# Kernel tuning notes

Measured on AMD Instinct MI355X. Metric: run time of the kernel, lower is better.

## Reference

```python
import jax, jax.numpy as jnp
import numpy as np

K = 3            # kernel size (hard-coded in CANCRB_Down: conv 3x3, stride 1, pad 1)
PAD = 1
S_CLUSTERS = 32  # cluster_num
KMEANS_ITERS = 8 # fixed Lloyd iterations (jit-friendly stand-in for the repo's kmeans)


def extract_patches(x):
    # x [B,C,H,W] -> [B,C,9,H,W] (3x3 neighborhoods, zero pad 1) == F.unfold layout
    B, C, H, W = x.shape
    xp = jnp.pad(x, ((0, 0), (0, 0), (PAD, PAD), (PAD, PAD)))
    return jnp.stack([xp[:, :, i:i + H, j:j + W] for i in range(K) for j in range(K)], axis=2)


def setup_inputs() -> dict:
    key = jax.random.key(0)
    ks = jax.random.split(key, 6)
    B, C, H, W = 8, 64, 128, 128
    O = C
    return {
        "x": jax.random.normal(ks[0], (B, C, H, W), jnp.float32),
        # LAGConv2D params: per-pixel 3x3 kernel-attention conv + base weight
        "att_w": jax.random.normal(ks[1], (K * K, C, K, K), jnp.float32) * 0.05,
        "att_b": jnp.zeros((K * K,), jnp.float32),
        "w1": jax.random.normal(ks[2], (O, C, K, K), jnp.float32) * (1.0 / np.sqrt(C * K * K)),
        "b1": jnp.zeros((O,), jnp.float32),
        # CANConv params: kernel generator (centroid patch -> 3x3 spatial attention) + base weight
        "kg_w": jax.random.normal(ks[3], (K * K, C * K * K), jnp.float32) * 0.02,
        "kg_b": jnp.zeros((K * K,), jnp.float32),
        "w2": jax.random.normal(ks[4], (O, C, K * K), jnp.float32) * (1.0 / np.sqrt(C * K * K)),
        "b2": jnp.zeros((O,), jnp.float32),
    }


def _lagconv(x, att_w, att_b, w1, b1):
    # local adaptive gating conv: per-pixel k*k attention modulates the shared kernel
    att = jax.nn.sigmoid(
        jax.lax.conv_general_dilated(x, att_w, (1, 1), "SAME") + att_b[None, :, None, None]
    )  # [B,9,H,W]
    p = extract_patches(x)  # [B,C,9,H,W]
    O, C = w1.shape[0], w1.shape[1]
    y = jnp.einsum('bckhw,bkhw,ock->bohw', p, att, w1.reshape(O, C, K * K))
    return y + b1[None, :, None, None]


def _kmeans_assign(feat, cent):
    # feat [B,N,C], cent [B,S,C] -> idx [B,N]; drop the ||feat||^2 constant
    d = jnp.sum(cent * cent, axis=-1)[:, None, :] - 2.0 * jnp.einsum('bnc,bsc->bns', feat, cent)
    return jnp.argmin(d, axis=-1)


def _kmeans(feat, S):
    B, N, C = feat.shape
    cent = feat[:, ::max(N // S, 1), :][:, :S, :]  # deterministic evenly-spaced init
    for _ in range(KMEANS_ITERS):
        idx = _kmeans_assign(feat, cent)
        oh = jax.nn.one_hot(idx, S, dtype=feat.dtype)          # [B,N,S]
        cnt = jnp.clip(jnp.sum(oh, axis=1), 1.0)               # [B,S]
        cent = jnp.einsum('bns,bnc->bsc', oh, feat) / cnt[..., None]
    return _kmeans_assign(feat, cent)


def _canconv(x, kg_w, kg_b, w2, b2, S):
    B, C, H, W = x.shape
    N = H * W
    feat = x.reshape(B, C, N).transpose(0, 2, 1)               # per-pixel channel features
    idx = _kmeans(feat, S)                                     # [B,N] cluster assignment
    p = extract_patches(x).reshape(B, C * K * K, N).transpose(0, 2, 1)  # [B,N,C*9]
    oh = jax.nn.one_hot(idx, S, dtype=x.dtype)
    cnt = jnp.clip(jnp.sum(oh, axis=1), 1.0)
    cent_p = jnp.einsum('bns,bnp->bsp', oh, p) / cnt[..., None]         # cluster mean patches
    # per-cluster 3x3 spatial attention; scaled softmax keeps kernel magnitude ~ base weight
    att = jax.nn.softmax(cent_p @ kg_w.T + kg_b, axis=-1) * float(K * K)  # [B,S,9]
    a_pix = jnp.take_along_axis(att, idx[..., None], axis=1)             # gather: [B,N,9]
    pm = p.reshape(B, N, C, K * K) * a_pix[:, :, None, :]
    y = jnp.einsum('bnck,ock->bno', pm, w2) + b2                          # [B,N,O]
    return y.transpose(0, 2, 1).reshape(B, w2.shape[0], H, W), idx


def reference(x, att_w, att_b, w1, b1, kg_w, kg_b, w2, b2):
    # NOTE: original torch forward overwrites `res` -- conv1+relu output is discarded.
    # We compute it for FLOP parity but it does not affect the output (faithful to the bug).
    _dead = jax.nn.relu(_lagconv(x, att_w, att_b, w1, b1))
    res, idx = _canconv(x, kg_w, kg_b, w2, b2, S_CLUSTERS)
    out = x + res
    return out, idx
```

## Files before the change

kernel.cpp:

```cpp
#include <hip/hip_runtime.h>
#include <hip/hip_bf16.h>

#define Bn 8
#define Cn 64
#define Np 16384
#define Sc 32
#define On 64
#define Dd 576
#define KM_ITERS 8
#define KMB 64
#define KBLK 32

typedef float f32x4 __attribute__((ext_vector_type(4)));
typedef __bf16 bf16x8 __attribute__((ext_vector_type(8)));
typedef __bf16 bf16x4 __attribute__((ext_vector_type(4)));

__device__ __forceinline__ void split3(float v, __bf16& h, __bf16& m, __bf16& lo) {
    h = (__bf16)v;
    float r = v - (float)h;
    m = (__bf16)r;
    lo = (__bf16)(r - (float)m);
}

__device__ __forceinline__ void split2(float v, __bf16& h, __bf16& m) {
    h = (__bf16)v;
    m = (__bf16)(v - (float)h);
}

__global__ __launch_bounds__(256) void featbf4_k(const float* __restrict__ x,
                                                 __bf16* __restrict__ fh,
                                                 __bf16* __restrict__ fm,
                                                 __bf16* __restrict__ xh,
                                                 __bf16* __restrict__ xm,
                                                 __bf16* __restrict__ xl) {
    __shared__ float tile[64][65];
    int b = blockIdx.y, n0 = blockIdx.x * 64, t = threadIdx.x;
    int j = t & 63, c0 = (t >> 6) * 16;
    #pragma unroll
    for (int cc = 0; cc < 16; ++cc)
        tile[c0 + cc][j] = x[((size_t)b * Cn + c0 + cc) * Np + n0 + j];
    __syncthreads();

    {
        int n_loc = t & 63, cq = (t >> 6) * 16;
        bf16x8 vh[2], vm[2];
        #pragma unroll
        for (int g = 0; g < 2; ++g)
            #pragma unroll
            for (int u = 0; u < 8; ++u) {
                __bf16 h, m;
                split2(tile[cq + g * 8 + u][n_loc], h, m);
                vh[g][u] = h; vm[g][u] = m;
            }
        size_t base = ((size_t)b * Np + n0 + n_loc) * Cn + cq;
        *(bf16x8*)&fh[base] = vh[0]; *(bf16x8*)&fh[base + 8] = vh[1];
        *(bf16x8*)&fm[base] = vm[0]; *(bf16x8*)&fm[base + 8] = vm[1];
    }
    {
        int c = t >> 2, jq = (t & 3) * 16;
        bf16x8 hh[2], mm2[2], ll[2];
        #pragma unroll
        for (int g = 0; g < 2; ++g)
            #pragma unroll
            for (int u = 0; u < 8; ++u) {
                __bf16 h, m, lo;
                split3(tile[c][jq + g * 8 + u], h, m, lo);
                hh[g][u] = h; mm2[g][u] = m; ll[g][u] = lo;
            }
        size_t cb = ((size_t)b * Cn + c) * Np + n0 + jq;
        *(bf16x8*)&xh[cb] = hh[0]; *(bf16x8*)&xh[cb + 8] = hh[1];
        *(bf16x8*)&xm[cb] = mm2[0]; *(bf16x8*)&xm[cb + 8] = mm2[1];
        *(bf16x8*)&xl[cb] = ll[0]; *(bf16x8*)&xl[cb + 8] = ll[1];
    }
}

__global__ __launch_bounds__(64) void init_cent3_k(const float* __restrict__ x,
                                                   float* __restrict__ cent_f32,
                                                   __bf16* __restrict__ ch_,
                                                   __bf16* __restrict__ cm_,
                                                   float* __restrict__ cnorm) {
    int b = blockIdx.y, s = blockIdx.x, c = threadIdx.x;
    int n = s * (Np / Sc);
    float v = x[((size_t)b * Cn + c) * Np + n];
    int o = (b * Sc + s) * Cn + c;
    cent_f32[o] = v;
    __bf16 h, m; split2(v, h, m);
    ch_[o] = h; cm_[o] = m;
    float sq = v * v;
    #pragma unroll
    for (int off = 32; off >= 1; off >>= 1) sq += __shfl_down(sq, off);
    if (c == 0) cnorm[b * Sc + s] = sq;
}

__global__ __launch_bounds__(256) void w2prep_k(const float* __restrict__ w2,
                                                __bf16* __restrict__ w2kg) {
    int i = blockIdx.x * 256 + threadIdx.x;
    int k = i >> 12, rem = i & 4095, o = rem >> 6, c = rem & 63;
    w2kg[i] = (__bf16)w2[o * Dd + c * 9 + k];
}

__global__ __launch_bounds__(256, 3) void kmeans_fused4_k(
        const float* __restrict__ x,
        const __bf16* __restrict__ fh, const __bf16* __restrict__ fm,
        const __bf16* __restrict__ xh, const __bf16* __restrict__ xm, const __bf16* __restrict__ xl,
        const float* __restrict__ cent_f32,
        const __bf16* __restrict__ ch_, const __bf16* __restrict__ cm_,
        const float* __restrict__ cnorm,
        int* __restrict__ idxg, float* __restrict__ gpart,
        float* __restrict__ out_idx, int do_update) {
    __shared__ __bf16 A_oh[32][264];
    __shared__ int idx_s[256];
    __shared__ int redint[4][32];
    __shared__ float centf_s[32][64];
    __shared__ float cnorm_s[32];
    int b = blockIdx.y, n0 = blockIdx.x * 256, t = threadIdx.x;
    int w = t >> 6, l = t & 63, arow = l & 15, kg = l >> 4;

    for (int i = t; i < Sc * Cn; i += 256) ((float*)centf_s)[i] = cent_f32[b * Sc * Cn + i];
    if (t < Sc) cnorm_s[t] = cnorm[b * Sc + t];

    bf16x8 cbh[2][2], cbm[2][2];
    #pragma unroll
    for (int st = 0; st < 2; ++st)
        #pragma unroll
        for (int kt = 0; kt < 2; ++kt) {
            size_t cb = (size_t)(b * Sc + st * 16 + arow) * Cn + kt * 32 + kg * 8;
            cbh[st][kt] = *(const bf16x8*)&ch_[cb];
            cbm[st][kt] = *(const bf16x8*)&cm_[cb];
        }
    float cn0 = cnorm[b * Sc + arow];
    float cn1 = cnorm[b * Sc + 16 + arow];

    f32x4 dacc[4][2];
    #pragma unroll
    for (int mt = 0; mt < 4; ++mt) {
        dacc[mt][0] = (f32x4){0.f, 0.f, 0.f, 0.f};
        dacc[mt][1] = (f32x4){0.f, 0.f, 0.f, 0.f};
    }
    #pragma unroll
    for (int mt = 0; mt < 4; ++mt) {
        size_t fb = ((size_t)b * Np + n0 + w * 64 + mt * 16 + arow) * Cn;
        bf16x8 ah[2], am2[2];
        #pragma unroll
        for (int kt = 0; kt < 2; ++kt) {
            ah[kt]  = *(const bf16x8*)&fh[fb + kt * 32 + kg * 8];
            am2[kt] = *(const bf16x8*)&fm[fb + kt * 32 + kg * 8];
        }
        #pragma unroll
        for (int st = 0; st < 2; ++st)
            #pragma unroll
            for (int kt = 0; kt < 2; ++kt) {
                dacc[mt][st] = __builtin_amdgcn_mfma_f32_16x16x32_bf16(ah[kt],  cbh[st][kt], dacc[mt][st], 0, 0, 0);
                dacc[mt][st] = __builtin_amdgcn_mfma_f32_16x16x32_bf16(ah[kt],  cbm[st][kt], dacc[mt][st], 0, 0, 0);
                dacc[mt][st] = __builtin_amdgcn_mfma_f32_16x16x32_bf16(am2[kt], cbh[st][kt], dacc[mt][st], 0, 0, 0);
                dacc[mt][st] = __builtin_amdgcn_mfma_f32_16x16x32_bf16(am2[kt], cbm[st][kt], dacc[mt][st], 0, 0, 0);
            }
    }
    __syncthreads();

    #pragma unroll
    for (int mt = 0; mt < 4; ++mt)
        #pragma unroll
        for (int r = 0; r < 4; ++r) {
            float dA = cn0 - 2.f * dacc[mt][0][r];
            float dB = cn1 - 2.f * dacc[mt][1][r];
            float d1, d2; int s1;
            if (dB < dA) { d1 = dB; s1 = arow + 16; d2 = dA; }
            else         { d1 = dA; s1 = arow;      d2 = dB; }
            #pragma unroll
            for (int mk = 1; mk < 16; mk <<= 1) {
                float d1o = __shfl_xor(d1, mk);
                int   s1o = __shfl_xor(s1, mk);
                float d2o = __shfl_xor(d2, mk);
                float big = fmaxf(d1, d1o);
                d2 = fminf(fminf(d2, d2o), big);
                if (d1o < d1 || (d1o == d1 && s1o < s1)) { d1 = d1o; s1 = s1o; }
            }
            int pix = w * 64 + mt * 16 + kg * 4 + r;
            bool writer = (arow == 0);
            if (writer) idx_s[pix] = s1;
            bool flag = writer && ((d2 - d1) < 0.02f);
            unsigned long long bal = __ballot(flag);
            while (bal) {
                int src = __ffsll(bal) - 1;
                bal &= bal - 1;
                int fp = w * 64 + mt * 16 + (src >> 4) * 4 + r;
                int n = n0 + fp;
                int s = l & 31, c0 = (l >> 5) * 32;
                float acc2 = 0.f;
                #pragma unroll 8
                for (int c = 0; c < 32; ++c)
                    acc2 = fmaf(x[((size_t)b * Cn + c0 + c) * Np + n], centf_s[s][c0 + c], acc2);
                acc2 += __shfl_xor(acc2, 32);
                float dd = cnorm_s[s] - 2.f * acc2;
                int ss = s;
                #pragma unroll
                for (int mk = 1; mk < 32; mk <<= 1) {
                    float ddo = __shfl_xor(dd, mk);
                    int   sso = __shfl_xor(ss, mk);
                    if (ddo < dd || (ddo == dd && sso < ss)) { dd = ddo; ss = sso; }
                }
                if (l == 0) idx_s[fp] = ss;
            }
        }
    __syncthreads();

    int best = idx_s[t];
    if (out_idx) {
        idxg[b * Np + n0 + t] = best;
        out_idx[b * Np + n0 + t] = (float)best;
    }
    if (!do_update) return;

    #pragma unroll 4
    for (int s = 0; s < Sc; ++s) {
        unsigned long long bal = __ballot(best == s);
        if (l == 0) redint[w][s] = __popcll(bal);
    }

    #pragma unroll
    for (int s = 0; s < Sc; ++s)
        A_oh[s][t] = (s == best) ? (__bf16)1.0f : (__bf16)0.0f;
    __syncthreads();

    f32x4 uacc[2];
    uacc[0] = (f32x4){0.f, 0.f, 0.f, 0.f};
    uacc[1] = (f32x4){0.f, 0.f, 0.f, 0.f};
    size_t xrow = ((size_t)b * Cn + (w * 16 + arow)) * Np + n0;
    for (int mc = 0; mc < 4; ++mc) {
        #pragma unroll
        for (int kh = 0; kh < 2; ++kh) {
            size_t off = xrow + mc * 64 + kh * 32 + kg * 8;
            bf16x8 bh  = *(const bf16x8*)&xh[off];
            bf16x8 bm2 = *(const bf16x8*)&xm[off];
            bf16x8 bl2 = *(const bf16x8*)&xl[off];
            #pragma unroll
            for (int smt = 0; smt < 2; ++smt) {
                bf16x8 af = *(const bf16x8*)&A_oh[smt * 16 + arow][mc * 64 + kh * 32 + kg * 8];
                uacc[smt] = __builtin_amdgcn_mfma_f32_16x16x32_bf16(af, bh,  uacc[smt], 0, 0, 0);
                uacc[smt] = __builtin_amdgcn_mfma_f32_16x16x32_bf16(af, bm2, uacc[smt], 0, 0, 0);
                uacc[smt] = __builtin_amdgcn_mfma_f32_16x16x32_bf16(af, bl2, uacc[smt], 0, 0, 0);
            }
        }
    }
    float* gp = &gpart[(size_t)(b * KMB + blockIdx.x) * (Sc * 65)];
    #pragma unroll
    for (int smt = 0; smt < 2; ++smt)
        #pragma unroll
        for (int r = 0; r < 4; ++r)
            gp[(smt * 16 + kg * 4 + r) * 65 + w * 16 + arow] = uacc[smt][r];
    if (t < Sc)
        gp[t * 65 + 64] = (float)(redint[0][t] + redint[1][t] + redint[2][t] + redint[3][t]);
}

__global__ __launch_bounds__(256) void update_reduce3_k(const float* __restrict__ gpart,
                                                        float* __restrict__ cent_f32,
                                                        __bf16* __restrict__ ch_,
                                                        __bf16* __restrict__ cm_,
                                                        float* __restrict__ cnorm) {
    __shared__ float psum[4][64];
    __shared__ float pcnt[4];
    int b = blockIdx.y, s = blockIdx.x, t = threadIdx.x;
    int w = t >> 6, c = t & 63;
    float sum = 0.f, cnt = 0.f;
    #pragma unroll 4
    for (int blk = w * 16; blk < w * 16 + 16; ++blk) {
        const float* g = &gpart[(size_t)(b * KMB + blk) * (Sc * 65) + s * 65];
        sum += g[c];
        if (c == 0) cnt += g[64];
    }
    psum[w][c] = sum;
    if (c == 0) pcnt[w] = cnt;
    __syncthreads();
    if (t < 64) {
        float m = psum[0][t] + psum[1][t] + psum[2][t] + psum[3][t];
        float ct = pcnt[0] + pcnt[1] + pcnt[2] + pcnt[3];
        float mean = m / fmaxf(ct, 1.f);
        int o = (b * Sc + s) * Cn + t;
        cent_f32[o] = mean;
        __bf16 h, mm; split2(mean, h, mm);
        ch_[o] = h; cm_[o] = mm;
        float sq = mean * mean;
        #pragma unroll
        for (int off = 32; off >= 1; off >>= 1) sq += __shfl_down(sq, off);
        if (t == 0) cnorm[b * Sc + s] = sq;
    }
}

__global__ __launch_bounds__(512) void centp_mfma2_k(const __bf16* __restrict__ xh,
                                                     const int* __restrict__ idxg,
                                                     float* __restrict__ partialP) {
    __shared__ __bf16 Amat[288 * 56];
    int b = blockIdx.y, kb = blockIdx.x, t = threadIdx.x;
    int w = t >> 6, l = t & 63;
    int wm = w >> 2, wn = w & 3;
    int arow = l & 15, kg = l >> 4;
    f32x4 acc[9];
    #pragma unroll
    for (int j = 0; j < 9; ++j) acc[j] = (f32x4){0.f, 0.f, 0.f, 0.f};

    int m_base = kb * 512;
    size_t xrow = ((size_t)b * Cn + wn * 16 + arow) * Np;
    for (int kt = 0; kt < 16; ++kt) {
        int m0 = m_base + kt * 32;
        #pragma unroll
        for (int j = 0; j < 9; ++j) {
            int i = t + 512 * j;
            int row = i >> 4, dc = i & 15;
            *(unsigned*)&Amat[row * 56 + dc * 2] = 0u;
        }
        __syncthreads();
        if (t < 288) {
            int m = t & 31, k = t >> 5;
            int mg = m0 + m, mh = mg >> 7, mw = mg & 127;
            int dh = k / 3 - 1, dw = k % 3 - 1;
            int nh = mh - dh, nw = mw - dw;
            if (((unsigned)nh < 128u) && ((unsigned)nw < 128u)) {
                int s = idxg[b * Np + (nh << 7) + nw];
                Amat[(s * 9 + k) * 56 + m] = (__bf16)1.0f;
            }
        }
        __syncthreads();
        bf16x8 bfrag = *(const bf16x8*)&xh[xrow + m0 + kg * 8];
        #pragma unroll
        for (int j = 0; j < 9; ++j) {
            int mt = wm * 9 + j;
            bf16x8 afrag = *(const bf16x8*)&Amat[(mt * 16 + arow) * 56 + kg * 8];
            acc[j] = __builtin_amdgcn_mfma_f32_16x16x32_bf16(afrag, bfrag, acc[j], 0, 0, 0);
        }
        __syncthreads();
    }
    float* P = partialP + (size_t)(b * KBLK + kb) * 288 * 64;
    #pragma unroll
    for (int j = 0; j < 9; ++j) {
        int R0 = (wm * 9 + j) * 16 + kg * 4;
        int col = wn * 16 + arow;
        #pragma unroll
        for (int r = 0; r < 4; ++r) P[(size_t)(R0 + r) * 64 + col] = acc[j][r];
    }
}

__global__ __launch_bounds__(576) void centp_att2_k(const float* __restrict__ partialP,
                                                    const int* __restrict__ idxg,
                                                    const float* __restrict__ kg_w,
                                                    const float* __restrict__ kg_b,
                                                    float* __restrict__ attb) {
    __shared__ float cpm[9][64];
    __shared__ float logit[9];
    __shared__ int   redint[9];
    __shared__ float cnt_sh;
    int b = blockIdx.y, s = blockIdx.x, t = threadIdx.x;
    int k = t >> 6, c = t & 63;

    float sum = 0.f;
    for (int kb = 0; kb < KBLK; ++kb)
        sum += partialP[((size_t)(b * KBLK + kb) * 288 + s * 9 + k) * 64 + c];

    int cloc = 0;
    for (int i = t; i < Np; i += 576) cloc += (idxg[b * Np + i] == s);
    #pragma unroll
    for (int off = 32; off >= 1; off >>= 1) cloc += __shfl_down(cloc, off);
    if ((t & 63) == 0) redint[k] = cloc;
    __syncthreads();
    if (t == 0) {
        int c2 = 0;
        #pragma unroll
        for (int j = 0; j < 9; ++j) c2 += redint[j];
        cnt_sh = fmaxf((float)c2, 1.f);
    }
    __syncthreads();
    cpm[k][c] = sum / cnt_sh;
    __syncthreads();

    float pr = 0.f;
    #pragma unroll
    for (int u = 0; u < 9; ++u)
        pr = fmaf(cpm[u][c], kg_w[k * Dd + c * 9 + u], pr);
    #pragma unroll
    for (int off = 32; off >= 1; off >>= 1) pr += __shfl_down(pr, off);
    if ((t & 63) == 0) logit[k] = pr + kg_b[k];
    __syncthreads();
    if (t == 0) {
        float mx = logit[0];
        #pragma unroll
        for (int jj = 1; jj < 9; ++jj) mx = fmaxf(mx, logit[jj]);
        float e[9], sm = 0.f;
        #pragma unroll
        for (int jj = 0; jj < 9; ++jj) { e[jj] = expf(logit[jj] - mx); sm += e[jj]; }
        #pragma unroll
        for (int jj = 0; jj < 9; ++jj) attb[(b * Sc + s) * 9 + jj] = e[jj] / sm * 9.f;
    }
}

__global__ __launch_bounds__(512, 4) void final_out5_k(const float* __restrict__ x,
                                                       const __bf16* __restrict__ fh,
                                                       const int* __restrict__ idxg,
                                                       const float* __restrict__ attb,
                                                       const __bf16* __restrict__ w2kg,
                                                       const float* __restrict__ b2,
                                                       float* __restrict__ out) {
    __shared__ __align__(16) char smem[46080];
    __shared__ float apix_t[9][132];
    __shared__ float b2s[64];
    __bf16 (*w2l)[64][72] = (__bf16 (*)[64][72])smem;
    float (*trans)[132]   = (float (*)[132])smem;

    int b = blockIdx.y, hh = blockIdx.x, n0 = hh * 128, t = threadIdx.x;
    int w = t >> 6, l = t & 63, arow = l & 15, kg = l >> 4;

    if (t < 128) {
        int s = idxg[b * Np + n0 + t];
        const float* ap = attb + (b * Sc + s) * 9;
        #pragma unroll
        for (int k = 0; k < 9; ++k) apix_t[k][t] = ap[k];
    } else if (t < 192) {
        b2s[t - 128] = b2[t - 128];
    }
    for (int q = t; q < 2560; q += 512) {
        int kk = q >> 9, rem = q & 511, o = rem >> 3, c0 = (rem & 7) * 8;
        *(bf16x8*)&w2l[kk][o][c0] = *(const bf16x8*)&w2kg[(size_t)kk * 4096 + o * 64 + c0];
    }
    __syncthreads();

    int px = w * 16 + arow;
    f32x4 acc[4];
    #pragma unroll
    for (int nt = 0; nt < 4; ++nt) acc[nt] = (f32x4){0.f, 0.f, 0.f, 0.f};

    #define K_BODY(k, kk)                                                                  \
    {                                                                                      \
        const int dh = (k) / 3 - 1, dw = (k) % 3 - 1;                                      \
        int h2 = hh + dh, wc = px + dw;                                                    \
        bool valid = ((unsigned)h2 < 128u) && ((unsigned)wc < 128u);                       \
        const __bf16* fr = fh + (((size_t)b * Np + (h2 << 7) + wc) << 6);                  \
        bf16x8 av0 = (bf16x8)(__bf16)0.0f, av1 = (bf16x8)(__bf16)0.0f;                     \
        if (valid) {                                                                       \
            av0 = *(const bf16x8*)&fr[kg * 8];                                             \
            av1 = *(const bf16x8*)&fr[32 + kg * 8];                                        \
        }                                                                                  \
        f32x4 a4 = *(const f32x4*)&apix_t[k][w * 16 + kg * 4];                             \
        f32x4 acck[4];                                                                     \
        _Pragma("unroll")                                                                  \
        for (int nt = 0; nt < 4; ++nt) {                                                   \
            bf16x8 bv0 = *(const bf16x8*)&w2l[kk][nt * 16 + arow][kg * 8];                 \
            bf16x8 bv1 = *(const bf16x8*)&w2l[kk][nt * 16 + arow][32 + kg * 8];            \
            acck[nt] = __builtin_amdgcn_mfma_f32_16x16x32_bf16(av0, bv0,                   \
                           (f32x4){0.f, 0.f, 0.f, 0.f}, 0, 0, 0);                          \
            acck[nt] = __builtin_amdgcn_mfma_f32_16x16x32_bf16(av1, bv1, acck[nt], 0, 0, 0);\
        }                                                                                  \
        _Pragma("unroll")                                                                  \
        for (int nt = 0; nt < 4; ++nt)                                                     \
            _Pragma("unroll")                                                              \
            for (int r = 0; r < 4; ++r)                                                    \
                acc[nt][r] = fmaf(a4[r], acck[nt][r], acc[nt][r]);                         \
    }

    K_BODY(0, 0) K_BODY(1, 1) K_BODY(2, 2) K_BODY(3, 3) K_BODY(4, 4)
    __syncthreads();
    for (int q = t; q < 2048; q += 512) {
        int kk = q >> 9, rem = q & 511, o = rem >> 3, c0 = (rem & 7) * 8;
        *(bf16x8*)&w2l[kk][o][c0] = *(const bf16x8*)&w2kg[(size_t)(kk + 5) * 4096 + o * 64 + c0];
    }
    __syncthreads();
    K_BODY(5, 0) K_BODY(6, 1) K_BODY(7, 2) K_BODY(8, 3)
    #undef K_BODY

    __syncthreads();
    #pragma unroll
    for (int nt = 0; nt < 4; ++nt)
        #pragma unroll
        for (int r = 0; r < 4; ++r)
            trans[nt * 16 + arow][w * 16 + kg * 4 + r] = acc[nt][r];
    __syncthreads();
    for (int i = t; i < 8192; i += 512) {
        int o = i >> 7, p2 = i & 127;
        size_t gi = ((size_t)b * On + o) * Np + n0 + p2;
        out[gi] = x[gi] + trans[o][p2] + b2s[o];
    }
}

extern "C" void kernel_launch(void* const* d_in, const int* in_sizes, int n_in,
                              void* d_out, int out_size, void* d_ws, size_t ws_size,
                              hipStream_t stream) {
    (void)in_sizes; (void)n_in; (void)out_size; (void)ws_size;
    const float* x    = (const float*)d_in[0];
    const float* kg_w = (const float*)d_in[5];
    const float* kg_b = (const float*)d_in[6];
    const float* w2   = (const float*)d_in[7];
    const float* b2   = (const float*)d_in[8];
    float* out = (float*)d_out;

    char* p = (char*)d_ws;
    __bf16* fh      = (__bf16*)p; p += (size_t)Bn * Np * Cn * 2;
    __bf16* fm      = (__bf16*)p; p += (size_t)Bn * Np * Cn * 2;
    __bf16* xh      = (__bf16*)p; p += (size_t)Bn * Np * Cn * 2;
    __bf16* xm      = (__bf16*)p; p += (size_t)Bn * Np * Cn * 2;
    __bf16* xl      = (__bf16*)p; p += (size_t)Bn * Np * Cn * 2;
    float*  cent_f32= (float*)p;  p += (size_t)Bn * Sc * Cn * 4;
    __bf16* ch_     = (__bf16*)p; p += (size_t)Bn * Sc * Cn * 2;
    __bf16* cm_     = (__bf16*)p; p += (size_t)Bn * Sc * Cn * 2;
    float*  cnorm   = (float*)p;  p += (size_t)Bn * Sc * 4;
    int*    idxg    = (int*)p;    p += (size_t)Bn * Np * 4;
    float*  gpart   = (float*)p;  p += (size_t)Bn * KMB * Sc * 65 * 4;
    float*  attb    = (float*)p;  p += (size_t)Bn * Sc * 9 * 4;
    __bf16* w2kg    = (__bf16*)p; p += (size_t)9 * On * Cn * 2;
    float*  partialP = (float*)xm;

    featbf4_k<<<dim3(Np / 64, Bn), 256, 0, stream>>>(x, fh, fm, xh, xm, xl);
    init_cent3_k<<<dim3(Sc, Bn), 64, 0, stream>>>(x, cent_f32, ch_, cm_, cnorm);
    w2prep_k<<<(On * Dd) / 256, 256, 0, stream>>>(w2, w2kg);

    for (int it = 0; it < KM_ITERS; ++it) {
        kmeans_fused4_k<<<dim3(KMB, Bn), 256, 0, stream>>>(
            x, fh, fm, xh, xm, xl, cent_f32, ch_, cm_, cnorm, idxg, gpart, nullptr, 1);
        update_reduce3_k<<<dim3(Sc, Bn), 256, 0, stream>>>(gpart, cent_f32, ch_, cm_, cnorm);
    }
    kmeans_fused4_k<<<dim3(KMB, Bn), 256, 0, stream>>>(
        x, fh, fm, xh, xm, xl, cent_f32, ch_, cm_, cnorm, idxg, gpart,
        out + (size_t)Bn * On * Np, 0);

    centp_mfma2_k<<<dim3(KBLK, Bn), 512, 0, stream>>>(xh, idxg, partialP);
    centp_att2_k<<<dim3(Sc, Bn), 576, 0, stream>>>(partialP, idxg, kg_w, kg_b, attb);

    final_out5_k<<<dim3(128, Bn), 512, 0, stream>>>(x, fh, idxg, attb, w2kg, b2, out);
}
```

Before: 412.9 us.

## Fuse k-means iterations into one persistent kernel with grid barriers

Replaces the 17 launches of assign and update kernels with a single persistent kernel of 256 blocks. Each block processes 512 pixels per iteration, holds the centroids in shared memory, and after a device-wide atomic barrier redundantly reduces all partial sums for its batch. The intent is to remove launch overhead and the global centroid round trips between iterations. The cost is a spin barrier that requires all 256 blocks to be co-resident, plus a redundant 64-way partial-sum reduction in every block.

```diff
diff --git a/kernel.cpp b/kernel.cpp
--- a/kernel.cpp
+++ b/kernel.cpp
@@ -8,8 +8,10 @@
 #define On 64
 #define Dd 576
 #define KM_ITERS 8
-#define KMB 64
 #define KBLK 32
+#define GP_STRIDE 2048
+#define GP_BUFSZ  (Bn * 64 * GP_STRIDE)
+#define GC_BUFSZ  (Bn * Sc * 64)
 
 typedef float f32x4 __attribute__((ext_vector_type(4)));
 typedef __bf16 bf16x8 __attribute__((ext_vector_type(8)));
@@ -74,24 +76,6 @@
     }
 }
 
-__global__ __launch_bounds__(64) void init_cent3_k(const float* __restrict__ x,
-                                                   float* __restrict__ cent_f32,
-                                                   __bf16* __restrict__ ch_,
-                                                   __bf16* __restrict__ cm_,
-                                                   float* __restrict__ cnorm) {
-    int b = blockIdx.y, s = blockIdx.x, c = threadIdx.x;
-    int n = s * (Np / Sc);
-    float v = x[((size_t)b * Cn + c) * Np + n];
-    int o = (b * Sc + s) * Cn + c;
-    cent_f32[o] = v;
-    __bf16 h, m; split2(v, h, m);
-    ch_[o] = h; cm_[o] = m;
-    float sq = v * v;
-    #pragma unroll
-    for (int off = 32; off >= 1; off >>= 1) sq += __shfl_down(sq, off);
-    if (c == 0) cnorm[b * Sc + s] = sq;
-}
-
 __global__ __launch_bounds__(256) void w2prep_k(const float* __restrict__ w2,
                                                 __bf16* __restrict__ w2kg) {
     int i = blockIdx.x * 256 + threadIdx.x;
@@ -99,191 +83,222 @@
     w2kg[i] = (__bf16)w2[o * Dd + c * 9 + k];
 }
 
-__global__ __launch_bounds__(256, 3) void kmeans_fused4_k(
+__device__ __forceinline__ void grid_barrier(unsigned* ctr) {
+    __threadfence();
+    __syncthreads();
+    if (threadIdx.x == 0) {
+        __hip_atomic_fetch_add(ctr, 1u, __ATOMIC_ACQ_REL, __HIP_MEMORY_SCOPE_AGENT);
+        unsigned v;
+        do {
+            __builtin_amdgcn_s_sleep(2);
+            v = __hip_atomic_load(ctr, __ATOMIC_ACQUIRE, __HIP_MEMORY_SCOPE_AGENT);
+        } while (v < 256u);
+    }
+    __syncthreads();
+    __threadfence();
+}
+
+__global__ __launch_bounds__(256) void kmeans_loop2_k(
         const float* __restrict__ x,
         const __bf16* __restrict__ fh, const __bf16* __restrict__ fm,
         const __bf16* __restrict__ xh, const __bf16* __restrict__ xm, const __bf16* __restrict__ xl,
-        const float* __restrict__ cent_f32,
-        const __bf16* __restrict__ ch_, const __bf16* __restrict__ cm_,
-        const float* __restrict__ cnorm,
-        int* __restrict__ idxg, float* __restrict__ gpart,
-        float* __restrict__ out_idx, int do_update) {
+        unsigned* __restrict__ bar,
+        float* __restrict__ gpart, float* __restrict__ gcnt,
+        int* __restrict__ idxg, float* __restrict__ out_idx) {
     __shared__ __bf16 A_oh[32][264];
-    __shared__ int idx_s[256];
-    __shared__ int redint[4][32];
+    __shared__ __bf16 chs[32][72];
+    __shared__ __bf16 cms[32][72];
     __shared__ float centf_s[32][64];
     __shared__ float cnorm_s[32];
-    int b = blockIdx.y, n0 = blockIdx.x * 256, t = threadIdx.x;
+    __shared__ int idx_s[512];
+    __shared__ int redint[4][32];
+
+    int gb = blockIdx.x;
+    int b = gb >> 5, blk2 = gb & 31;
+    int t = threadIdx.x;
     int w = t >> 6, l = t & 63, arow = l & 15, kg = l >> 4;
 
-    for (int i = t; i < Sc * Cn; i += 256) ((float*)centf_s)[i] = cent_f32[b * Sc * Cn + i];
-    if (t < Sc) cnorm_s[t] = cnorm[b * Sc + t];
-
-    bf16x8 cbh[2][2], cbm[2][2];
-    #pragma unroll
-    for (int st = 0; st < 2; ++st)
-        #pragma unroll
-        for (int kt = 0; kt < 2; ++kt) {
-            size_t cb = (size_t)(b * Sc + st * 16 + arow) * Cn + kt * 32 + kg * 8;
-            cbh[st][kt] = *(const bf16x8*)&ch_[cb];
-            cbm[st][kt] = *(const bf16x8*)&cm_[cb];
+    #pragma unroll
+    for (int j = 0; j < 8; ++j) {
+        int s = w * 8 + j;
+        float v = x[((size_t)b * Cn + l) * Np + s * (Np / Sc)];
+        centf_s[s][l] = v;
+        __bf16 h, m; split2(v, h, m);
+        chs[s][l] = h; cms[s][l] = m;
+        float sq = v * v;
+        #pragma unroll
+        for (int off = 32; off >= 1; off >>= 1) sq += __shfl_down(sq, off);
+        if (l == 0) cnorm_s[s] = sq;
+    }
+    __syncthreads();
+
+    for (int it = 0; it <= KM_ITERS; ++it) {
+        bool last = (it == KM_ITERS);
+        size_t par  = (size_t)(it & 1) * GP_BUFSZ;
+        size_t parc = (size_t)(it & 1) * GC_BUFSZ;
+
+        for (int ts = 0; ts < 2; ++ts) {
+            int n0 = blk2 * 512 + ts * 256;
+            int ib = ts * 256;
+            int bk = blk2 * 2 + ts;
+
+            bf16x8 cbh[2][2], cbm[2][2];
+            #pragma unroll
+            for (int st = 0; st < 2; ++st)
+                #pragma unroll
+                for (int kt = 0; kt < 2; ++kt) {
+                    cbh[st][kt] = *(const bf16x8*)&chs[st * 16 + arow][kt * 32 + kg * 8];
+                    cbm[st][kt] = *(const bf16x8*)&cms[st * 16 + arow][kt * 32 + kg * 8];
+                }
+            float cn0 = cnorm_s[arow];
+            float cn1 = cnorm_s[16 + arow];
+
+            f32x4 dacc[4][2];
+            #pragma unroll
+            for (int mt = 0; mt < 4; ++mt) {
+                dacc[mt][0] = (f32x4){0.f, 0.f, 0.f, 0.f};
+                dacc[mt][1] = (f32x4){0.f, 0.f, 0.f, 0.f};
+            }
+            #pragma unroll
+            for (int mt = 0; mt < 4; ++mt) {
+                size_t fb = ((size_t)b * Np + n0 + w * 64 + mt * 16 + arow) * Cn;
+                bf16x8 ah[2], am2[2];
+                #pragma unroll
+                for (int kt = 0; kt < 2; ++kt) {
+                    ah[kt]  = *(const bf16x8*)&fh[fb + kt * 32 + kg * 8];
+                    am2[kt] = *(const bf16x8*)&fm[fb + kt * 32 + kg * 8];
+                }
+                #pragma unroll
+                for (int st = 0; st < 2; ++st)
+                    #pragma unroll
+                    for (int kt = 0; kt < 2; ++kt) {
+                        dacc[mt][st] = __builtin_amdgcn_mfma_f32_16x16x32_bf16(ah[kt],  cbh[st][kt], dacc[mt][st], 0, 0, 0);
+                        dacc[mt][st] = __builtin_amdgcn_mfma_f32_16x16x32_bf16(ah[kt],  cbm[st][kt], dacc[mt][st], 0, 0, 0);
+                        dacc[mt][st] = __builtin_amdgcn_mfma_f32_16x16x32_bf16(am2[kt], cbh[st][kt], dacc[mt][st], 0, 0, 0);
+                        dacc[mt][st] = __builtin_amdgcn_mfma_f32_16x16x32_bf16(am2[kt], cbm[st][kt], dacc[mt][st], 0, 0, 0);
+                    }
+            }
+
+            #pragma unroll
+            for (int mt = 0; mt < 4; ++mt)
+                #pragma unroll
+                for (int r = 0; r < 4; ++r) {
+                    float dA = cn0 - 2.f * dacc[mt][0][r];
+                    float dB = cn1 - 2.f * dacc[mt][1][r];
+                    float d1, d2; int s1;
+                    if (dB < dA) { d1 = dB; s1 = arow + 16; d2 = dA; }
+                    else         { d1 = dA; s1 = arow;      d2 = dB; }
+                    #pragma unroll
+                    for (int mk = 1; mk < 16; mk <<= 1) {
+                        float d1o = __shfl_xor(d1, mk);
+                        int   s1o = __shfl_xor(s1, mk);
+                        float d2o = __shfl_xor(d2, mk);
+                        float big = fmaxf(d1, d1o);
+                        d2 = fminf(fminf(d2, d2o), big);
+                        if (d1o < d1 || (d1o == d1 && s1o < s1)) { d1 = d1o; s1 = s1o; }
+                    }
+                    int pix = w * 64 + mt * 16 + kg * 4 + r;
+                    bool writer = (arow == 0);
+                    if (writer) idx_s[ib + pix] = s1;
+                    bool flag = writer && ((d2 - d1) < 0.02f);
+                    unsigned long long bal = __ballot(flag);
+                    while (bal) {
+                        int src = __ffsll(bal) - 1;
+                        bal &= bal - 1;
+                        int fp = w * 64 + mt * 16 + (src >> 4) * 4 + r;
+                        int n = n0 + fp;
+                        int s = l & 31, c0 = (l >> 5) * 32;
+                        float acc2 = 0.f;
+                        #pragma unroll 8
+                        for (int c = 0; c < 32; ++c)
+                            acc2 = fmaf(x[((size_t)b * Cn + c0 + c) * Np + n], centf_s[s][c0 + c], acc2);
+                        acc2 += __shfl_xor(acc2, 32);
+                        float dd = cnorm_s[s] - 2.f * acc2;
+                        int ss = s;
+                        #pragma unroll
+                        for (int mk = 1; mk < 32; mk <<= 1) {
+                            float ddo = __shfl_xor(dd, mk);
+                            int   sso = __shfl_xor(ss, mk);
+                            if (ddo < dd || (ddo == dd && sso < ss)) { dd = ddo; ss = sso; }
+                        }
+                        if (l == 0) idx_s[ib + fp] = ss;
+                    }
+                }
+            __syncthreads();
+
+            int best = idx_s[ib + t];
+            if (last) {
+                idxg[b * Np + n0 + t] = best;
+                out_idx[b * Np + n0 + t] = (float)best;
+                continue;
+            }
+
+            #pragma unroll 4
+            for (int s = 0; s < Sc; ++s) {
+                unsigned long long bal = __ballot(best == s);
+                if (l == 0) redint[w][s] = __popcll(bal);
+            }
+            __syncthreads();
+
+            #pragma unroll
+            for (int s = 0; s < Sc; ++s)
+                A_oh[s][t] = (s == best) ? (__bf16)1.0f : (__bf16)0.0f;
+            __syncthreads();
+
+            f32x4 uacc[2];
+            uacc[0] = (f32x4){0.f, 0.f, 0.f, 0.f};
+            uacc[1] = (f32x4){0.f, 0.f, 0.f, 0.f};
+            size_t xrow = ((size_t)b * Cn + (w * 16 + arow)) * Np + n0;
+            for (int mc = 0; mc < 4; ++mc) {
+                #pragma unroll
+                for (int kh = 0; kh < 2; ++kh) {
+                    size_t off = xrow + mc * 64 + kh * 32 + kg * 8;
+                    bf16x8 bh  = *(const bf16x8*)&xh[off];
+                    bf16x8 bm2 = *(const bf16x8*)&xm[off];
+                    bf16x8 bl2 = *(const bf16x8*)&xl[off];
+                    #pragma unroll
+                    for (int smt = 0; smt < 2; ++smt) {
+                        bf16x8 af = *(const bf16x8*)&A_oh[smt * 16 + arow][mc * 64 + kh * 32 + kg * 8];
+                        uacc[smt] = __builtin_amdgcn_mfma_f32_16x16x32_bf16(af, bh,  uacc[smt], 0, 0, 0);
+                        uacc[smt] = __builtin_amdgcn_mfma_f32_16x16x32_bf16(af, bm2, uacc[smt], 0, 0, 0);
+                        uacc[smt] = __builtin_amdgcn_mfma_f32_16x16x32_bf16(af, bl2, uacc[smt], 0, 0, 0);
+                    }
+                }
+            }
+            float* gp = gpart + par + (size_t)(b * 64 + bk) * GP_STRIDE;
+            #pragma unroll
+            for (int smt = 0; smt < 2; ++smt)
+                #pragma unroll
+                for (int r = 0; r < 4; ++r)
+                    gp[(smt * 16 + kg * 4 + r) * 64 + w * 16 + arow] = uacc[smt][r];
+            if (t < Sc)
+                gcnt[parc + (size_t)(b * Sc + t) * 64 + bk] =
+                    (float)(redint[0][t] + redint[1][t] + redint[2][t] + redint[3][t]);
         }
-    float cn0 = cnorm[b * Sc + arow];
-    float cn1 = cnorm[b * Sc + 16 + arow];
-
-    f32x4 dacc[4][2];
-    #pragma unroll
-    for (int mt = 0; mt < 4; ++mt) {
-        dacc[mt][0] = (f32x4){0.f, 0.f, 0.f, 0.f};
-        dacc[mt][1] = (f32x4){0.f, 0.f, 0.f, 0.f};
-    }
-    #pragma unroll
-    for (int mt = 0; mt < 4; ++mt) {
-        size_t fb = ((size_t)b * Np + n0 + w * 64 + mt * 16 + arow) * Cn;
-        bf16x8 ah[2], am2[2];
-        #pragma unroll
-        for (int kt = 0; kt < 2; ++kt) {
-            ah[kt]  = *(const bf16x8*)&fh[fb + kt * 32 + kg * 8];
-            am2[kt] = *(const bf16x8*)&fm[fb + kt * 32 + kg * 8];
+        if (last) break;
+
+        grid_barrier(&bar[it]);
+
+        const float* gp0 = gpart + par + (size_t)b * 64 * GP_STRIDE;
+        #pragma unroll 2
+        for (int j = 0; j < 8; ++j) {
+            int s = w * 8 + j;
+            float sum = 0.f;
+            for (int bk2 = 0; bk2 < 64; ++bk2)
+                sum += gp0[(size_t)bk2 * GP_STRIDE + s * 64 + l];
+            float cnt = gcnt[parc + (size_t)(b * Sc + s) * 64 + l];
+            #pragma unroll
+            for (int off = 32; off >= 1; off >>= 1) cnt += __shfl_xor(cnt, off);
+            float mean = sum / fmaxf(cnt, 1.f);
+            centf_s[s][l] = mean;
+            __bf16 h, m; split2(mean, h, m);
+            chs[s][l] = h; cms[s][l] = m;
+            float sq = mean * mean;
+            #pragma unroll
+            for (int off = 32; off >= 1; off >>= 1) sq += __shfl_down(sq, off);
+            if (l == 0) cnorm_s[s] = sq;
         }
-        #pragma unroll
-        for (int st = 0; st < 2; ++st)
-            #pragma unroll
-            for (int kt = 0; kt < 2; ++kt) {
-                dacc[mt][st] = __builtin_amdgcn_mfma_f32_16x16x32_bf16(ah[kt],  cbh[st][kt], dacc[mt][st], 0, 0, 0);
-                dacc[mt][st] = __builtin_amdgcn_mfma_f32_16x16x32_bf16(ah[kt],  cbm[st][kt], dacc[mt][st], 0, 0, 0);
-                dacc[mt][st] = __builtin_amdgcn_mfma_f32_16x16x32_bf16(am2[kt], cbh[st][kt], dacc[mt][st], 0, 0, 0);
-                dacc[mt][st] = __builtin_amdgcn_mfma_f32_16x16x32_bf16(am2[kt], cbm[st][kt], dacc[mt][st], 0, 0, 0);
-            }
-    }
-    __syncthreads();
-
-    #pragma unroll
-    for (int mt = 0; mt < 4; ++mt)
-        #pragma unroll
-        for (int r = 0; r < 4; ++r) {
-            float dA = cn0 - 2.f * dacc[mt][0][r];
-            float dB = cn1 - 2.f * dacc[mt][1][r];
-            float d1, d2; int s1;
-            if (dB < dA) { d1 = dB; s1 = arow + 16; d2 = dA; }
-            else         { d1 = dA; s1 = arow;      d2 = dB; }
-            #pragma unroll
-            for (int mk = 1; mk < 16; mk <<= 1) {
-                float d1o = __shfl_xor(d1, mk);
-                int   s1o = __shfl_xor(s1, mk);
-                float d2o = __shfl_xor(d2, mk);
-                float big = fmaxf(d1, d1o);
-                d2 = fminf(fminf(d2, d2o), big);
-                if (d1o < d1 || (d1o == d1 && s1o < s1)) { d1 = d1o; s1 = s1o; }
-            }
-            int pix = w * 64 + mt * 16 + kg * 4 + r;
-            bool writer = (arow == 0);
-            if (writer) idx_s[pix] = s1;
-            bool flag = writer && ((d2 - d1) < 0.02f);
-            unsigned long long bal = __ballot(flag);
-            while (bal) {
-                int src = __ffsll(bal) - 1;
-                bal &= bal - 1;
-                int fp = w * 64 + mt * 16 + (src >> 4) * 4 + r;
-                int n = n0 + fp;
-                int s = l & 31, c0 = (l >> 5) * 32;
-                float acc2 = 0.f;
-                #pragma unroll 8
-                for (int c = 0; c < 32; ++c)
-                    acc2 = fmaf(x[((size_t)b * Cn + c0 + c) * Np + n], centf_s[s][c0 + c], acc2);
-                acc2 += __shfl_xor(acc2, 32);
-                float dd = cnorm_s[s] - 2.f * acc2;
-                int ss = s;
-                #pragma unroll
-                for (int mk = 1; mk < 32; mk <<= 1) {
-                    float ddo = __shfl_xor(dd, mk);
-                    int   sso = __shfl_xor(ss, mk);
-                    if (ddo < dd || (ddo == dd && sso < ss)) { dd = ddo; ss = sso; }
-                }
-                if (l == 0) idx_s[fp] = ss;
-            }
-        }
-    __syncthreads();
-
-    int best = idx_s[t];
-    if (out_idx) {
-        idxg[b * Np + n0 + t] = best;
-        out_idx[b * Np + n0 + t] = (float)best;
-    }
-    if (!do_update) return;
-
-    #pragma unroll 4
-    for (int s = 0; s < Sc; ++s) {
-        unsigned long long bal = __ballot(best == s);
-        if (l == 0) redint[w][s] = __popcll(bal);
-    }
-
-    #pragma unroll
-    for (int s = 0; s < Sc; ++s)
-        A_oh[s][t] = (s == best) ? (__bf16)1.0f : (__bf16)0.0f;
-    __syncthreads();
-
-    f32x4 uacc[2];
-    uacc[0] = (f32x4){0.f, 0.f, 0.f, 0.f};
-    uacc[1] = (f32x4){0.f, 0.f, 0.f, 0.f};
-    size_t xrow = ((size_t)b * Cn + (w * 16 + arow)) * Np + n0;
-    for (int mc = 0; mc < 4; ++mc) {
-        #pragma unroll
-        for (int kh = 0; kh < 2; ++kh) {
-            size_t off = xrow + mc * 64 + kh * 32 + kg * 8;
-            bf16x8 bh  = *(const bf16x8*)&xh[off];
-            bf16x8 bm2 = *(const bf16x8*)&xm[off];
-            bf16x8 bl2 = *(const bf16x8*)&xl[off];
-            #pragma unroll
-            for (int smt = 0; smt < 2; ++smt) {
-                bf16x8 af = *(const bf16x8*)&A_oh[smt * 16 + arow][mc * 64 + kh * 32 + kg * 8];
-                uacc[smt] = __builtin_amdgcn_mfma_f32_16x16x32_bf16(af, bh,  uacc[smt], 0, 0, 0);
-                uacc[smt] = __builtin_amdgcn_mfma_f32_16x16x32_bf16(af, bm2, uacc[smt], 0, 0, 0);
-                uacc[smt] = __builtin_amdgcn_mfma_f32_16x16x32_bf16(af, bl2, uacc[smt], 0, 0, 0);
-            }
-        }
-    }
-    float* gp = &gpart[(size_t)(b * KMB + blockIdx.x) * (Sc * 65)];
-    #pragma unroll
-    for (int smt = 0; smt < 2; ++smt)
-        #pragma unroll
-        for (int r = 0; r < 4; ++r)
-            gp[(smt * 16 + kg * 4 + r) * 65 + w * 16 + arow] = uacc[smt][r];
-    if (t < Sc)
-        gp[t * 65 + 64] = (float)(redint[0][t] + redint[1][t] + redint[2][t] + redint[3][t]);
-}
-
-__global__ __launch_bounds__(256) void update_reduce3_k(const float* __restrict__ gpart,
-                                                        float* __restrict__ cent_f32,
-                                                        __bf16* __restrict__ ch_,
-                                                        __bf16* __restrict__ cm_,
-                                                        float* __restrict__ cnorm) {
-    __shared__ float psum[4][64];
-    __shared__ float pcnt[4];
-    int b = blockIdx.y, s = blockIdx.x, t = threadIdx.x;
-    int w = t >> 6, c = t & 63;
-    float sum = 0.f, cnt = 0.f;
-    #pragma unroll 4
-    for (int blk = w * 16; blk < w * 16 + 16; ++blk) {
-        const float* g = &gpart[(size_t)(b * KMB + blk) * (Sc * 65) + s * 65];
-        sum += g[c];
-        if (c == 0) cnt += g[64];
-    }
-    psum[w][c] = sum;
-    if (c == 0) pcnt[w] = cnt;
-    __syncthreads();
-    if (t < 64) {
-        float m = psum[0][t] + psum[1][t] + psum[2][t] + psum[3][t];
-        float ct = pcnt[0] + pcnt[1] + pcnt[2] + pcnt[3];
-        float mean = m / fmaxf(ct, 1.f);
-        int o = (b * Sc + s) * Cn + t;
-        cent_f32[o] = mean;
-        __bf16 h, mm; split2(mean, h, mm);
-        ch_[o] = h; cm_[o] = mm;
-        float sq = mean * mean;
-        #pragma unroll
-        for (int off = 32; off >= 1; off >>= 1) sq += __shfl_down(sq, off);
-        if (t == 0) cnorm[b * Sc + s] = sq;
+        __syncthreads();
     }
 }
 
@@ -491,33 +506,26 @@
     float* out = (float*)d_out;
 
     char* p = (char*)d_ws;
+    unsigned* bar   = (unsigned*)p; p += 256;
     __bf16* fh      = (__bf16*)p; p += (size_t)Bn * Np * Cn * 2;
     __bf16* fm      = (__bf16*)p; p += (size_t)Bn * Np * Cn * 2;
     __bf16* xh      = (__bf16*)p; p += (size_t)Bn * Np * Cn * 2;
     __bf16* xm      = (__bf16*)p; p += (size_t)Bn * Np * Cn * 2;
     __bf16* xl      = (__bf16*)p; p += (size_t)Bn * Np * Cn * 2;
-    float*  cent_f32= (float*)p;  p += (size_t)Bn * Sc * Cn * 4;
-    __bf16* ch_     = (__bf16*)p; p += (size_t)Bn * Sc * Cn * 2;
-    __bf16* cm_     = (__bf16*)p; p += (size_t)Bn * Sc * Cn * 2;
-    float*  cnorm   = (float*)p;  p += (size_t)Bn * Sc * 4;
+    float*  gpart   = (float*)p;  p += (size_t)2 * GP_BUFSZ * 4;
+    float*  gcnt    = (float*)p;  p += (size_t)2 * GC_BUFSZ * 4;
     int*    idxg    = (int*)p;    p += (size_t)Bn * Np * 4;
-    float*  gpart   = (float*)p;  p += (size_t)Bn * KMB * Sc * 65 * 4;
     float*  attb    = (float*)p;  p += (size_t)Bn * Sc * 9 * 4;
     __bf16* w2kg    = (__bf16*)p; p += (size_t)9 * On * Cn * 2;
     float*  partialP = (float*)xm;
 
+    hipMemsetAsync(bar, 0, 256, stream);
+
     featbf4_k<<<dim3(Np / 64, Bn), 256, 0, stream>>>(x, fh, fm, xh, xm, xl);
-    init_cent3_k<<<dim3(Sc, Bn), 64, 0, stream>>>(x, cent_f32, ch_, cm_, cnorm);
     w2prep_k<<<(On * Dd) / 256, 256, 0, stream>>>(w2, w2kg);
 
-    for (int it = 0; it < KM_ITERS; ++it) {
-        kmeans_fused4_k<<<dim3(KMB, Bn), 256, 0, stream>>>(
-            x, fh, fm, xh, xm, xl, cent_f32, ch_, cm_, cnorm, idxg, gpart, nullptr, 1);
-        update_reduce3_k<<<dim3(Sc, Bn), 256, 0, stream>>>(gpart, cent_f32, ch_, cm_, cnorm);
-    }
-    kmeans_fused4_k<<<dim3(KMB, Bn), 256, 0, stream>>>(
-        x, fh, fm, xh, xm, xl, cent_f32, ch_, cm_, cnorm, idxg, gpart,
-        out + (size_t)Bn * On * Np, 0);
+    kmeans_loop2_k<<<256, 256, 0, stream>>>(x, fh, fm, xh, xm, xl, bar, gpart, gcnt,
+                                            idxg, out + (size_t)Bn * On * Np);
 
     centp_mfma2_k<<<dim3(KBLK, Bn), 512, 0, stream>>>(xh, idxg, partialP);
     centp_att2_k<<<dim3(Sc, Bn), 576, 0, stream>>>(partialP, idxg, kg_w, kg_b, attb);
```

New measurement: 1.126 ms. 173% more time.
